# Kernel tuning notes

Hardware: AMD Instinct MI355X
Metric: run time of the kernel (lower is better)

The kernel has to match this reference:

```python
import jax, jax.numpy as jnp
import numpy as np

EMBED = 1024
HEADS = 16
HDIM = 64
FFN = 4 * EMBED
EPS = 1e-5


def setup_inputs() -> dict:
    key = jax.random.key(0)
    ks = jax.random.split(key, 12)
    def lin(k, fan_in, shape):
        b = 1.0 / np.sqrt(fan_in)
        return jax.random.uniform(k, shape, jnp.float32, -b, b)
    return {
        "x": jax.random.normal(ks[0], (4, 2048, EMBED), jnp.float32),
        "Wq": lin(ks[1], EMBED, (EMBED, HEADS * HDIM)),
        "Wk": lin(ks[2], EMBED, (EMBED, HEADS * HDIM)),
        "Wv": lin(ks[3], EMBED, (EMBED, HEADS * HDIM)),
        "Wo": lin(ks[4], HEADS * HDIM, (HEADS * HDIM, EMBED)),
        "ln1_g": jnp.ones((EMBED,), jnp.float32),
        "ln1_b": jnp.zeros((EMBED,), jnp.float32),
        "ln2_g": jnp.ones((EMBED,), jnp.float32),
        "ln2_b": jnp.zeros((EMBED,), jnp.float32),
        "W1": lin(ks[5], EMBED, (EMBED, FFN)),
        "b1": lin(ks[6], EMBED, (FFN,)),
        "W2": lin(ks[7], FFN, (FFN, EMBED)),
        "b2": lin(ks[8], FFN, (EMBED,)),
    }


def _layer_norm(x, g, b):
    mu = jnp.mean(x, axis=-1, keepdims=True)
    var = jnp.var(x, axis=-1, keepdims=True)
    return (x - mu) * jax.lax.rsqrt(var + EPS) * g + b


def reference(x, Wq, Wk, Wv, Wo, ln1_g, ln1_b, ln2_g, ln2_b, W1, b1, W2, b2):
    B, S, _ = x.shape
    residual = x
    h = _layer_norm(x, ln1_g, ln1_b)
    # project and split heads: [B, H, S, Dh]
    q = (h @ Wq).reshape(B, S, HEADS, HDIM).transpose(0, 2, 1, 3)
    k = (h @ Wk).reshape(B, S, HEADS, HDIM).transpose(0, 2, 1, 3)
    v = (h @ Wv).reshape(B, S, HEADS, HDIM).transpose(0, 2, 1, 3)
    scale = HDIM ** -0.5
    scores = jnp.einsum("bhqd,bhkd->bhqk", q, k) * scale
    # causal mask (upper triangle excluded above diagonal -> -inf)
    mask = jnp.triu(jnp.ones((S, S), bool), k=1)
    scores = jnp.where(mask, -jnp.inf, scores)
    attn = jax.nn.softmax(scores, axis=-1)
    out = jnp.einsum("bhqk,bhkd->bhqd", attn, v)
    out = out.transpose(0, 2, 1, 3).reshape(B, S, HEADS * HDIM)
    x = residual + out @ Wo
    residual = x
    h = _layer_norm(x, ln2_g, ln2_b)
    h = jax.nn.gelu(h @ W1 + b1, approximate=False) @ W2 + b2
    return residual + h
```

## Files before the change

kernel.cpp:

```cpp
#include <hip/hip_runtime.h>
#include <hip/hip_bf16.h>
#include <math.h>

typedef __bf16 bf16;
typedef bf16 bf16x8 __attribute__((ext_vector_type(8)));
typedef bf16 bf16x4 __attribute__((ext_vector_type(4)));
typedef float f32x4 __attribute__((ext_vector_type(4)));

#define ROWS 8192
#define EMB  1024
#define NH   16
#define HD   64
#define FFN  4096
#define QKVN 3072
#define SEQ  2048

__device__ __forceinline__ void gl2lds16(const bf16* g, bf16* l) {
  __builtin_amdgcn_global_load_lds((const __attribute__((address_space(1))) void*)g,
                                   (__attribute__((address_space(3))) void*)l, 16, 0, 0);
}

__global__ void transpose_cast(const float* __restrict__ W, bf16* __restrict__ Wt,
                               int K, int N, float scale) {
  __shared__ float tile[32][33];
  const int n0 = blockIdx.x * 32, k0 = blockIdx.y * 32;
  const int tx = threadIdx.x & 31, ty = threadIdx.x >> 5;
#pragma unroll
  for (int i = 0; i < 32; i += 8)
    tile[ty + i][tx] = W[(size_t)(k0 + ty + i) * N + n0 + tx];
  __syncthreads();
#pragma unroll
  for (int i = 0; i < 32; i += 8)
    Wt[(size_t)(n0 + ty + i) * K + k0 + tx] = (bf16)(tile[tx][ty + i] * scale);
}

__global__ void transpose_cast4(const float* __restrict__ W0, const float* __restrict__ W1,
                                const float* __restrict__ W2, const float* __restrict__ W3,
                                bf16* __restrict__ dst) {
  __shared__ float tile[32][33];
  const int z = blockIdx.z;
  const float* W = (z == 0) ? W0 : (z == 1) ? W1 : (z == 2) ? W2 : W3;
  const float scale = (z == 0) ? 0.125f : 1.0f;
  bf16* Wt = dst + (size_t)z * EMB * EMB;
  const int n0 = blockIdx.x * 32, k0 = blockIdx.y * 32;
  const int tx = threadIdx.x & 31, ty = threadIdx.x >> 5;
#pragma unroll
  for (int i = 0; i < 32; i += 8)
    tile[ty + i][tx] = W[(size_t)(k0 + ty + i) * EMB + n0 + tx];
  __syncthreads();
#pragma unroll
  for (int i = 0; i < 32; i += 8)
    Wt[(size_t)(n0 + ty + i) * EMB + k0 + tx] = (bf16)(tile[tx][ty + i] * scale);
}

__global__ void v_transpose(const bf16* __restrict__ qkv, bf16* __restrict__ vt) {
  __shared__ bf16 tile[32][33];
  const int s0 = blockIdx.x * 32, d0 = blockIdx.y * 32, bh = blockIdx.z;
  const int b = bh >> 4, h = bh & 15;
  const int tx = threadIdx.x & 31, ty = threadIdx.x >> 5;
#pragma unroll
  for (int i = 0; i < 32; i += 8)
    tile[ty + i][tx] = qkv[(size_t)(b * SEQ + s0 + ty + i) * QKVN + 2 * EMB + h * HD + d0 + tx];
  __syncthreads();
#pragma unroll
  for (int i = 0; i < 32; i += 8)
    vt[(size_t)(bh * HD + d0 + ty + i) * SEQ + s0 + tx] = tile[tx][ty + i];
}

__global__ __launch_bounds__(256) void layernorm_bf16(
    const float* __restrict__ x, const float* __restrict__ g,
    const float* __restrict__ b, bf16* __restrict__ out) {
  const int row = blockIdx.x * 4 + (threadIdx.x >> 6);
  const int lane = threadIdx.x & 63;
  const float4* xr = (const float4*)(x + (size_t)row * EMB);
  float4 v[4];
  float s = 0.f, ss = 0.f;
#pragma unroll
  for (int k = 0; k < 4; k++) {
    v[k] = xr[lane + 64 * k];
    s += v[k].x + v[k].y + v[k].z + v[k].w;
    ss += v[k].x * v[k].x + v[k].y * v[k].y + v[k].z * v[k].z + v[k].w * v[k].w;
  }
#pragma unroll
  for (int off = 32; off; off >>= 1) {
    s += __shfl_xor(s, off);
    ss += __shfl_xor(ss, off);
  }
  const float mu = s * (1.0f / EMB);
  const float rs = rsqrtf(ss * (1.0f / EMB) - mu * mu + 1e-5f);
  bf16* orow = out + (size_t)row * EMB;
#pragma unroll
  for (int k = 0; k < 4; k++) {
    const float4 gv = ((const float4*)g)[lane + 64 * k];
    const float4 bv = ((const float4*)b)[lane + 64 * k];
    bf16x4 o;
    o[0] = (bf16)((v[k].x - mu) * rs * gv.x + bv.x);
    o[1] = (bf16)((v[k].y - mu) * rs * gv.y + bv.y);
    o[2] = (bf16)((v[k].z - mu) * rs * gv.z + bv.z);
    o[3] = (bf16)((v[k].w - mu) * rs * gv.w + bv.w);
    *(bf16x4*)(orow + (size_t)(lane + 64 * k) * 4) = o;
  }
}

template <int EPI, int N_, int K_>
__global__ __launch_bounds__(256, 2) void gemm_bt(
    const bf16* __restrict__ A, const bf16* __restrict__ Bt, void* __restrict__ C,
    const float* __restrict__ bias, const float* __restrict__ resid) {
  constexpr int N = N_, K = K_;
  __shared__ __align__(16) bf16 As[128 * 64];
  __shared__ __align__(16) bf16 Bs[128 * 64];
  const int tid = threadIdx.x;
  const int lane = tid & 63;
  const int wave = tid >> 6;
  const int wm = (wave >> 1) * 64;
  const int wn = (wave & 1) * 64;
  constexpr int tn = N / 128;
  const int lin = blockIdx.y * tn + blockIdx.x;
  const int xcd = lin & 7;
  const int idx = lin >> 3;
  const int m0 = (xcd * 8 + (idx & 7)) * 128;
  const int n0 = (idx >> 3) * 128;
  const int quad = lane >> 4;
  const int l16 = lane & 15;
  const int srow8 = lane >> 3;
  const int scol = ((lane & 7) ^ srow8) * 8;
  const int xr = l16 & 7;

  const bf16* ap = A + (size_t)(m0 + wave * 32 + srow8) * K + scol;
  const bf16* bp = Bt + (size_t)(n0 + wave * 32 + srow8) * K + scol;
  bf16* const as0 = &As[wave * 32 * 64];
  bf16* const bs0 = &Bs[wave * 32 * 64];

  f32x4 acc[4][4] = {};

  for (int kt = 0; kt < K; kt += 64) {
    __syncthreads();
#pragma unroll
    for (int q = 0; q < 4; q++) {
      gl2lds16(ap + q * 8 * K, as0 + q * 8 * 64);
      gl2lds16(bp + q * 8 * K, bs0 + q * 8 * 64);
    }
    ap += 64;
    bp += 64;
    __syncthreads();
#pragma unroll
    for (int h = 0; h < 2; h++) {
      const int cp = ((h * 4 + quad) ^ xr) * 8;
      bf16x8 af[4], bfr[4];
#pragma unroll
      for (int i = 0; i < 4; i++)
        af[i] = *(const bf16x8*)&As[(wm + i * 16 + l16) * 64 + cp];
#pragma unroll
      for (int j = 0; j < 4; j++)
        bfr[j] = *(const bf16x8*)&Bs[(wn + j * 16 + l16) * 64 + cp];
#pragma unroll
      for (int i = 0; i < 4; i++)
#pragma unroll
        for (int j = 0; j < 4; j++)
          acc[i][j] = __builtin_amdgcn_mfma_f32_16x16x32_bf16(af[i], bfr[j], acc[i][j], 0, 0, 0);
    }
  }

#pragma unroll
  for (int i = 0; i < 4; i++)
#pragma unroll
    for (int j = 0; j < 4; j++)
#pragma unroll
      for (int r = 0; r < 4; r++) {
        const int row = m0 + wm + i * 16 + quad * 4 + r;
        const int col = n0 + wn + j * 16 + l16;
        const size_t idx2 = (size_t)row * N + col;
        float v = acc[i][j][r];
        if (EPI == 0) {
          ((bf16*)C)[idx2] = (bf16)v;
        } else if (EPI == 1) {
          ((float*)C)[idx2] = v + resid[idx2];
        } else if (EPI == 2) {
          v += bias[col];
          const float u = 1.5957691216f * (v + 0.044715f * v * v * v);
          v = v / (1.0f + __expf(-u));
          ((bf16*)C)[idx2] = (bf16)v;
        } else {
          ((float*)C)[idx2] = v + bias[col] + resid[idx2];
        }
      }
}

__global__ __launch_bounds__(256, 6) void flash_attn(
    const bf16* __restrict__ qkv, const bf16* __restrict__ vt, bf16* __restrict__ out) {
  const int bid = blockIdx.x;
  const int xcd = bid & 7;
  const int idx = bid >> 3;
  const int qt = 31 - (idx & 31);
  const int bh = xcd + ((idx >> 5) << 3);
  const int b = bh >> 4, h = bh & 15;
  const int tid = threadIdx.x;
  const int lane = tid & 63, wave = tid >> 6;
  const int quad = lane >> 4, l16 = lane & 15;

  __shared__ __align__(16) bf16 Ks[64 * 64];
  __shared__ __align__(16) bf16 Vts[64 * 64];
  __shared__ __align__(16) bf16 Ps[4][16][72];

  const size_t rowbase = (size_t)b * SEQ;
  const int s8 = (lane >> 3) & 7;
  const int cs = ((lane & 7) ^ s8) * 8;
  const int xk = l16 & 7;
  const bf16* kbase = qkv + rowbase * QKVN + EMB + h * HD;
  const bf16* vbase = vt + (size_t)(bh * HD) * SEQ;

  const int qrow_a = qt * 64 + wave * 16 + l16;
  const bf16* qptr = qkv + (rowbase + qrow_a) * QKVN + h * HD;
  const bf16x8 qf0 = *(const bf16x8*)(qptr + quad * 8);
  const bf16x8 qf1 = *(const bf16x8*)(qptr + 32 + quad * 8);
  f32x4 o0 = {}, o1 = {}, o2 = {}, o3 = {};
  f32x4 lsum = {};
  const int qrow_c = qt * 64 + wave * 16 + quad * 4;

  const bf16* kp = kbase + (size_t)(wave * 8 + s8) * QKVN + cs;
  const bf16* vp = vbase + (size_t)(wave * 8 + s8) * SEQ + cs;

#pragma unroll 1
  for (int kt = 0; kt <= qt; kt++) {
    __syncthreads();
    gl2lds16(kp + (size_t)kt * 64 * QKVN, &Ks[(wave * 8) * 64]);
    gl2lds16(kp + (size_t)(kt * 64 + 32) * QKVN, &Ks[(32 + wave * 8) * 64]);
    gl2lds16(vp + kt * 64, &Vts[(wave * 8) * 64]);
    gl2lds16(vp + (size_t)32 * SEQ + kt * 64, &Vts[(32 + wave * 8) * 64]);
    __syncthreads();

    if (kt < qt) {
#pragma unroll
      for (int j = 0; j < 4; j++) {
        const int rr = (j * 16 + l16) * 64;
        const bf16x8 kf0 = *(const bf16x8*)&Ks[rr + (quad ^ xk) * 8];
        const bf16x8 kf1 = *(const bf16x8*)&Ks[rr + ((4 + quad) ^ xk) * 8];
        f32x4 a = {};
        a = __builtin_amdgcn_mfma_f32_16x16x32_bf16(qf0, kf0, a, 0, 0, 0);
        a = __builtin_amdgcn_mfma_f32_16x16x32_bf16(qf1, kf1, a, 0, 0, 0);
#pragma unroll
        for (int r = 0; r < 4; r++) {
          const float pj = __expf(a[r]);
          lsum[r] += pj;
          Ps[wave][quad * 4 + r][j * 16 + l16] = (bf16)pj;
        }
      }
    } else {
#pragma unroll
      for (int j = 0; j < 4; j++) {
        if (j > wave) {
#pragma unroll
          for (int r = 0; r < 4; r++)
            Ps[wave][quad * 4 + r][j * 16 + l16] = (bf16)0.0f;
        } else {
          const int rr = (j * 16 + l16) * 64;
          const bf16x8 kf0 = *(const bf16x8*)&Ks[rr + (quad ^ xk) * 8];
          const bf16x8 kf1 = *(const bf16x8*)&Ks[rr + ((4 + quad) ^ xk) * 8];
          f32x4 a = {};
          a = __builtin_amdgcn_mfma_f32_16x16x32_bf16(qf0, kf0, a, 0, 0, 0);
          a = __builtin_amdgcn_mfma_f32_16x16x32_bf16(qf1, kf1, a, 0, 0, 0);
          if (j == wave) {
#pragma unroll
            for (int r = 0; r < 4; r++) {
              const float v = (l16 > quad * 4 + r) ? -INFINITY : a[r];
              const float pj = __expf(v);
              lsum[r] += pj;
              Ps[wave][quad * 4 + r][j * 16 + l16] = (bf16)pj;
            }
          } else {
#pragma unroll
            for (int r = 0; r < 4; r++) {
              const float pj = __expf(a[r]);
              lsum[r] += pj;
              Ps[wave][quad * 4 + r][j * 16 + l16] = (bf16)pj;
            }
          }
        }
      }
    }

    const bf16x8 af0 = *(const bf16x8*)&Ps[wave][l16][quad * 8];
    const bf16x8 af1 = *(const bf16x8*)&Ps[wave][l16][32 + quad * 8];
#pragma unroll
    for (int j = 0; j < 4; j++) {
      const int rr = (j * 16 + l16) * 64;
      const bf16x8 vf0 = *(const bf16x8*)&Vts[rr + (quad ^ xk) * 8];
      const bf16x8 vf1 = *(const bf16x8*)&Vts[rr + ((4 + quad) ^ xk) * 8];
      f32x4& oj = (j == 0) ? o0 : (j == 1) ? o1 : (j == 2) ? o2 : o3;
      oj = __builtin_amdgcn_mfma_f32_16x16x32_bf16(af0, vf0, oj, 0, 0, 0);
      oj = __builtin_amdgcn_mfma_f32_16x16x32_bf16(af1, vf1, oj, 0, 0, 0);
    }
  }

#pragma unroll
  for (int r = 0; r < 4; r++) {
    float ls = lsum[r];
    ls += __shfl_xor(ls, 1);
    ls += __shfl_xor(ls, 2);
    ls += __shfl_xor(ls, 4);
    ls += __shfl_xor(ls, 8);
    const float iv = 1.0f / ls;
    bf16* op = out + (rowbase + qrow_c + r) * EMB + h * HD;
    op[0 + l16] = (bf16)(o0[r] * iv);
    op[16 + l16] = (bf16)(o1[r] * iv);
    op[32 + l16] = (bf16)(o2[r] * iv);
    op[48 + l16] = (bf16)(o3[r] * iv);
  }
}

extern "C" void kernel_launch(void* const* d_in, const int* in_sizes, int n_in,
                              void* d_out, int out_size, void* d_ws, size_t ws_size,
                              hipStream_t stream) {
  const float* x     = (const float*)d_in[0];
  const float* Wq    = (const float*)d_in[1];
  const float* Wk    = (const float*)d_in[2];
  const float* Wv    = (const float*)d_in[3];
  const float* Wo    = (const float*)d_in[4];
  const float* ln1_g = (const float*)d_in[5];
  const float* ln1_b = (const float*)d_in[6];
  const float* ln2_g = (const float*)d_in[7];
  const float* ln2_b = (const float*)d_in[8];
  const float* W1    = (const float*)d_in[9];
  const float* b1    = (const float*)d_in[10];
  const float* W2    = (const float*)d_in[11];
  const float* b2    = (const float*)d_in[12];
  float* out = (float*)d_out;

  bf16* p = (bf16*)d_ws;
  bf16* wqkv_t = p;                 p += (size_t)QKVN * EMB;
  bf16* wo_t   = p;                 p += (size_t)EMB * EMB;
  bf16* w1_t   = p;                 p += (size_t)FFN * EMB;
  bf16* w2_t   = p;                 p += (size_t)EMB * FFN;
  bf16* h      = p;                 p += (size_t)ROWS * EMB;
  bf16* qkv    = p;                 p += (size_t)ROWS * QKVN;
  bf16* attn_o = p;                 p += (size_t)ROWS * EMB;
  bf16* ffn1   = p;
  bf16* vt     = h;

  transpose_cast4<<<dim3(32, 32, 4), 256, 0, stream>>>(Wq, Wk, Wv, Wo, wqkv_t);
  transpose_cast<<<dim3(128, 32), 256, 0, stream>>>(W1, w1_t, EMB, FFN, 1.0f);
  transpose_cast<<<dim3(32, 128), 256, 0, stream>>>(W2, w2_t, FFN, EMB, 1.0f);

  layernorm_bf16<<<ROWS / 4, 256, 0, stream>>>(x, ln1_g, ln1_b, h);

  gemm_bt<0, QKVN, EMB><<<dim3(QKVN / 128, ROWS / 128), 256, 0, stream>>>(
      h, wqkv_t, qkv, nullptr, nullptr);

  v_transpose<<<dim3(SEQ / 32, HD / 32, 64), 256, 0, stream>>>(qkv, vt);

  flash_attn<<<2048, 256, 0, stream>>>(qkv, vt, attn_o);

  gemm_bt<1, EMB, EMB><<<dim3(EMB / 128, ROWS / 128), 256, 0, stream>>>(
      attn_o, wo_t, out, nullptr, x);

  layernorm_bf16<<<ROWS / 4, 256, 0, stream>>>(out, ln2_g, ln2_b, h);

  gemm_bt<2, FFN, EMB><<<dim3(FFN / 128, ROWS / 128), 256, 0, stream>>>(
      h, w1_t, ffn1, b1, nullptr);

  gemm_bt<3, EMB, FFN><<<dim3(EMB / 128, ROWS / 128), 256, 0, stream>>>(
      ffn1, w2_t, out, b2, out);
}
```

Measured before the change: 481.0 us.

## Pair causal q-tiles per block, double-buffer K in LDS, read V from global

Each attention block now processes two query tiles (qt and 31-qt) so every block does a balanced amount of causal work, and the grid is halved accordingly. K tiles are double-buffered in LDS with the next tile prefetched while the current one is used. V fragments are loaded directly from global memory instead of being staged in LDS. This aims to remove tail imbalance and load stalls, at the risk of uncoalesced, latency-bound V reads and fewer resident blocks.

```diff
diff --git a/kernel.cpp b/kernel.cpp
--- a/kernel.cpp
+++ b/kernel.cpp
@@ -191,15 +191,14 @@
   const int bid = blockIdx.x;
   const int xcd = bid & 7;
   const int idx = bid >> 3;
-  const int qt = 31 - (idx & 31);
-  const int bh = xcd + ((idx >> 5) << 3);
+  const int pr = idx & 15;
+  const int bh = xcd + ((idx >> 4) << 3);
   const int b = bh >> 4, h = bh & 15;
   const int tid = threadIdx.x;
   const int lane = tid & 63, wave = tid >> 6;
   const int quad = lane >> 4, l16 = lane & 15;
 
-  __shared__ __align__(16) bf16 Ks[64 * 64];
-  __shared__ __align__(16) bf16 Vts[64 * 64];
+  __shared__ __align__(16) bf16 Ks[2][64 * 64];
   __shared__ __align__(16) bf16 Ps[4][16][72];
 
   const size_t rowbase = (size_t)b * SEQ;
@@ -209,103 +208,115 @@
   const bf16* kbase = qkv + rowbase * QKVN + EMB + h * HD;
   const bf16* vbase = vt + (size_t)(bh * HD) * SEQ;
 
-  const int qrow_a = qt * 64 + wave * 16 + l16;
-  const bf16* qptr = qkv + (rowbase + qrow_a) * QKVN + h * HD;
-  const bf16x8 qf0 = *(const bf16x8*)(qptr + quad * 8);
-  const bf16x8 qf1 = *(const bf16x8*)(qptr + 32 + quad * 8);
-  f32x4 o0 = {}, o1 = {}, o2 = {}, o3 = {};
-  f32x4 lsum = {};
-  const int qrow_c = qt * 64 + wave * 16 + quad * 4;
-
   const bf16* kp = kbase + (size_t)(wave * 8 + s8) * QKVN + cs;
-  const bf16* vp = vbase + (size_t)(wave * 8 + s8) * SEQ + cs;
+
+#define STAGE_K(BUF, T)                                                        \
+  gl2lds16(kp + (size_t)(T) * 64 * QKVN, &Ks[(BUF)][(wave * 8) * 64]);         \
+  gl2lds16(kp + ((size_t)(T) * 64 + 32) * QKVN, &Ks[(BUF)][(32 + wave * 8) * 64]);
 
 #pragma unroll 1
-  for (int kt = 0; kt <= qt; kt++) {
-    __syncthreads();
-    gl2lds16(kp + (size_t)kt * 64 * QKVN, &Ks[(wave * 8) * 64]);
-    gl2lds16(kp + (size_t)(kt * 64 + 32) * QKVN, &Ks[(32 + wave * 8) * 64]);
-    gl2lds16(vp + kt * 64, &Vts[(wave * 8) * 64]);
-    gl2lds16(vp + (size_t)32 * SEQ + kt * 64, &Vts[(32 + wave * 8) * 64]);
-    __syncthreads();
-
-    if (kt < qt) {
-#pragma unroll
-      for (int j = 0; j < 4; j++) {
-        const int rr = (j * 16 + l16) * 64;
-        const bf16x8 kf0 = *(const bf16x8*)&Ks[rr + (quad ^ xk) * 8];
-        const bf16x8 kf1 = *(const bf16x8*)&Ks[rr + ((4 + quad) ^ xk) * 8];
-        f32x4 a = {};
-        a = __builtin_amdgcn_mfma_f32_16x16x32_bf16(qf0, kf0, a, 0, 0, 0);
-        a = __builtin_amdgcn_mfma_f32_16x16x32_bf16(qf1, kf1, a, 0, 0, 0);
-#pragma unroll
-        for (int r = 0; r < 4; r++) {
-          const float pj = __expf(a[r]);
-          lsum[r] += pj;
-          Ps[wave][quad * 4 + r][j * 16 + l16] = (bf16)pj;
-        }
-      }
-    } else {
-#pragma unroll
-      for (int j = 0; j < 4; j++) {
-        if (j > wave) {
-#pragma unroll
-          for (int r = 0; r < 4; r++)
-            Ps[wave][quad * 4 + r][j * 16 + l16] = (bf16)0.0f;
-        } else {
+  for (int half = 0; half < 2; half++) {
+    const int qt = half ? pr : 31 - pr;
+    const int qrow_a = qt * 64 + wave * 16 + l16;
+    const bf16* qptr = qkv + (rowbase + qrow_a) * QKVN + h * HD;
+    const bf16x8 qf0 = *(const bf16x8*)(qptr + quad * 8);
+    const bf16x8 qf1 = *(const bf16x8*)(qptr + 32 + quad * 8);
+    f32x4 o0 = {}, o1 = {}, o2 = {}, o3 = {};
+    f32x4 lsum = {};
+    const int qrow_c = qt * 64 + wave * 16 + quad * 4;
+
+    STAGE_K(0, 0);
+    asm volatile("s_waitcnt vmcnt(0)");
+    __builtin_amdgcn_s_barrier();
+
+#pragma unroll 1
+    for (int kt = 0; kt <= qt; kt++) {
+      const int cb = kt & 1;
+      if (kt < qt) { STAGE_K(cb ^ 1, kt + 1); }
+      const bf16* Kc = &Ks[cb][0];
+
+      if (kt < qt) {
+#pragma unroll
+        for (int j = 0; j < 4; j++) {
           const int rr = (j * 16 + l16) * 64;
-          const bf16x8 kf0 = *(const bf16x8*)&Ks[rr + (quad ^ xk) * 8];
-          const bf16x8 kf1 = *(const bf16x8*)&Ks[rr + ((4 + quad) ^ xk) * 8];
+          const bf16x8 kf0 = *(const bf16x8*)&Kc[rr + (quad ^ xk) * 8];
+          const bf16x8 kf1 = *(const bf16x8*)&Kc[rr + ((4 + quad) ^ xk) * 8];
           f32x4 a = {};
           a = __builtin_amdgcn_mfma_f32_16x16x32_bf16(qf0, kf0, a, 0, 0, 0);
           a = __builtin_amdgcn_mfma_f32_16x16x32_bf16(qf1, kf1, a, 0, 0, 0);
-          if (j == wave) {
-#pragma unroll
-            for (int r = 0; r < 4; r++) {
-              const float v = (l16 > quad * 4 + r) ? -INFINITY : a[r];
-              const float pj = __expf(v);
-              lsum[r] += pj;
-              Ps[wave][quad * 4 + r][j * 16 + l16] = (bf16)pj;
-            }
+#pragma unroll
+          for (int r = 0; r < 4; r++) {
+            const float pj = __expf(a[r]);
+            lsum[r] += pj;
+            Ps[wave][quad * 4 + r][j * 16 + l16] = (bf16)pj;
+          }
+        }
+      } else {
+#pragma unroll
+        for (int j = 0; j < 4; j++) {
+          if (j > wave) {
+#pragma unroll
+            for (int r = 0; r < 4; r++)
+              Ps[wave][quad * 4 + r][j * 16 + l16] = (bf16)0.0f;
           } else {
-#pragma unroll
-            for (int r = 0; r < 4; r++) {
-              const float pj = __expf(a[r]);
-              lsum[r] += pj;
-              Ps[wave][quad * 4 + r][j * 16 + l16] = (bf16)pj;
+            const int rr = (j * 16 + l16) * 64;
+            const bf16x8 kf0 = *(const bf16x8*)&Kc[rr + (quad ^ xk) * 8];
+            const bf16x8 kf1 = *(const bf16x8*)&Kc[rr + ((4 + quad) ^ xk) * 8];
+            f32x4 a = {};
+            a = __builtin_amdgcn_mfma_f32_16x16x32_bf16(qf0, kf0, a, 0, 0, 0);
+            a = __builtin_amdgcn_mfma_f32_16x16x32_bf16(qf1, kf1, a, 0, 0, 0);
+            if (j == wave) {
+#pragma unroll
+              for (int r = 0; r < 4; r++) {
+                const float v = (l16 > quad * 4 + r) ? -INFINITY : a[r];
+                const float pj = __expf(v);
+                lsum[r] += pj;
+                Ps[wave][quad * 4 + r][j * 16 + l16] = (bf16)pj;
+              }
+            } else {
+#pragma unroll
+              for (int r = 0; r < 4; r++) {
+                const float pj = __expf(a[r]);
+                lsum[r] += pj;
+                Ps[wave][quad * 4 + r][j * 16 + l16] = (bf16)pj;
+              }
             }
           }
         }
       }
+
+      const bf16x8 af0 = *(const bf16x8*)&Ps[wave][l16][quad * 8];
+      const bf16x8 af1 = *(const bf16x8*)&Ps[wave][l16][32 + quad * 8];
+#pragma unroll
+      for (int j = 0; j < 4; j++) {
+        const bf16* vrow = vbase + (size_t)(j * 16 + l16) * SEQ + kt * 64;
+        const bf16x8 vf0 = *(const bf16x8*)(vrow + quad * 8);
+        const bf16x8 vf1 = *(const bf16x8*)(vrow + 32 + quad * 8);
+        f32x4& oj = (j == 0) ? o0 : (j == 1) ? o1 : (j == 2) ? o2 : o3;
+        oj = __builtin_amdgcn_mfma_f32_16x16x32_bf16(af0, vf0, oj, 0, 0, 0);
+        oj = __builtin_amdgcn_mfma_f32_16x16x32_bf16(af1, vf1, oj, 0, 0, 0);
+      }
+
+      asm volatile("s_waitcnt vmcnt(0)");
+      __builtin_amdgcn_s_barrier();
     }
 
-    const bf16x8 af0 = *(const bf16x8*)&Ps[wave][l16][quad * 8];
-    const bf16x8 af1 = *(const bf16x8*)&Ps[wave][l16][32 + quad * 8];
-#pragma unroll
-    for (int j = 0; j < 4; j++) {
-      const int rr = (j * 16 + l16) * 64;
-      const bf16x8 vf0 = *(const bf16x8*)&Vts[rr + (quad ^ xk) * 8];
-      const bf16x8 vf1 = *(const bf16x8*)&Vts[rr + ((4 + quad) ^ xk) * 8];
-      f32x4& oj = (j == 0) ? o0 : (j == 1) ? o1 : (j == 2) ? o2 : o3;
-      oj = __builtin_amdgcn_mfma_f32_16x16x32_bf16(af0, vf0, oj, 0, 0, 0);
-      oj = __builtin_amdgcn_mfma_f32_16x16x32_bf16(af1, vf1, oj, 0, 0, 0);
+#pragma unroll
+    for (int r = 0; r < 4; r++) {
+      float ls = lsum[r];
+      ls += __shfl_xor(ls, 1);
+      ls += __shfl_xor(ls, 2);
+      ls += __shfl_xor(ls, 4);
+      ls += __shfl_xor(ls, 8);
+      const float iv = 1.0f / ls;
+      bf16* op = out + (rowbase + qrow_c + r) * EMB + h * HD;
+      op[0 + l16] = (bf16)(o0[r] * iv);
+      op[16 + l16] = (bf16)(o1[r] * iv);
+      op[32 + l16] = (bf16)(o2[r] * iv);
+      op[48 + l16] = (bf16)(o3[r] * iv);
     }
   }
-
-#pragma unroll
-  for (int r = 0; r < 4; r++) {
-    float ls = lsum[r];
-    ls += __shfl_xor(ls, 1);
-    ls += __shfl_xor(ls, 2);
-    ls += __shfl_xor(ls, 4);
-    ls += __shfl_xor(ls, 8);
-    const float iv = 1.0f / ls;
-    bf16* op = out + (rowbase + qrow_c + r) * EMB + h * HD;
-    op[0 + l16] = (bf16)(o0[r] * iv);
-    op[16 + l16] = (bf16)(o1[r] * iv);
-    op[32 + l16] = (bf16)(o2[r] * iv);
-    op[48 + l16] = (bf16)(o3[r] * iv);
-  }
+#undef STAGE_K
 }
 
 extern "C" void kernel_launch(void* const* d_in, const int* in_sizes, int n_in,
@@ -348,7 +359,7 @@
 
   v_transpose<<<dim3(SEQ / 32, HD / 32, 64), 256, 0, stream>>>(qkv, vt);
 
-  flash_attn<<<2048, 256, 0, stream>>>(qkv, vt, attn_o);
+  flash_attn<<<1024, 256, 0, stream>>>(qkv, vt, attn_o);
 
   gemm_bt<1, EMB, EMB><<<dim3(EMB / 128, ROWS / 128), 256, 0, stream>>>(
       attn_o, wo_t, out, nullptr, x);
```

New measurement: 511.8 us. +6.4%, slower.

## Pair causal query tiles per block and register-prefetch next K/V tile

Applied to the files above, without the earlier changes.

Each flash-attention block now processes two query tiles (qt and 31-qt) so every block does equal causal work, halving the grid. K/V loads switch from direct global-to-LDS copies to register staging, and the next tile is loaded while the current one is computed, overlapping global latency with MFMA work. The cost is higher register pressure and fewer blocks, which may reduce occupancy and tail parallelism.

```diff
diff --git a/kernel.cpp b/kernel.cpp
--- a/kernel.cpp
+++ b/kernel.cpp
@@ -191,8 +191,8 @@
   const int bid = blockIdx.x;
   const int xcd = bid & 7;
   const int idx = bid >> 3;
-  const int qt = 31 - (idx & 31);
-  const int bh = xcd + ((idx >> 5) << 3);
+  const int pr = idx & 15;
+  const int bh = xcd + ((idx >> 4) << 3);
   const int b = bh >> 4, h = bh & 15;
   const int tid = threadIdx.x;
   const int lane = tid & 63, wave = tid >> 6;
@@ -209,103 +209,125 @@
   const bf16* kbase = qkv + rowbase * QKVN + EMB + h * HD;
   const bf16* vbase = vt + (size_t)(bh * HD) * SEQ;
 
-  const int qrow_a = qt * 64 + wave * 16 + l16;
-  const bf16* qptr = qkv + (rowbase + qrow_a) * QKVN + h * HD;
-  const bf16x8 qf0 = *(const bf16x8*)(qptr + quad * 8);
-  const bf16x8 qf1 = *(const bf16x8*)(qptr + 32 + quad * 8);
-  f32x4 o0 = {}, o1 = {}, o2 = {}, o3 = {};
-  f32x4 lsum = {};
-  const int qrow_c = qt * 64 + wave * 16 + quad * 4;
-
   const bf16* kp = kbase + (size_t)(wave * 8 + s8) * QKVN + cs;
   const bf16* vp = vbase + (size_t)(wave * 8 + s8) * SEQ + cs;
+  bf16* const kd0 = &Ks[(wave * 8) * 64 + lane * 8];
+  bf16* const kd1 = &Ks[(32 + wave * 8) * 64 + lane * 8];
+  bf16* const vd0 = &Vts[(wave * 8) * 64 + lane * 8];
+  bf16* const vd1 = &Vts[(32 + wave * 8) * 64 + lane * 8];
+
+  bf16x8 rk0, rk1, rv0, rv1;
+#define LOAD_KV(T)                                                             \
+  rk0 = *(const bf16x8*)(kp + (size_t)(T) * 64 * QKVN);                        \
+  rk1 = *(const bf16x8*)(kp + ((size_t)(T) * 64 + 32) * QKVN);                 \
+  rv0 = *(const bf16x8*)(vp + (T) * 64);                                       \
+  rv1 = *(const bf16x8*)(vp + (size_t)32 * SEQ + (T) * 64);
 
 #pragma unroll 1
-  for (int kt = 0; kt <= qt; kt++) {
-    __syncthreads();
-    gl2lds16(kp + (size_t)kt * 64 * QKVN, &Ks[(wave * 8) * 64]);
-    gl2lds16(kp + (size_t)(kt * 64 + 32) * QKVN, &Ks[(32 + wave * 8) * 64]);
-    gl2lds16(vp + kt * 64, &Vts[(wave * 8) * 64]);
-    gl2lds16(vp + (size_t)32 * SEQ + kt * 64, &Vts[(32 + wave * 8) * 64]);
-    __syncthreads();
-
-    if (kt < qt) {
-#pragma unroll
-      for (int j = 0; j < 4; j++) {
-        const int rr = (j * 16 + l16) * 64;
-        const bf16x8 kf0 = *(const bf16x8*)&Ks[rr + (quad ^ xk) * 8];
-        const bf16x8 kf1 = *(const bf16x8*)&Ks[rr + ((4 + quad) ^ xk) * 8];
-        f32x4 a = {};
-        a = __builtin_amdgcn_mfma_f32_16x16x32_bf16(qf0, kf0, a, 0, 0, 0);
-        a = __builtin_amdgcn_mfma_f32_16x16x32_bf16(qf1, kf1, a, 0, 0, 0);
-#pragma unroll
-        for (int r = 0; r < 4; r++) {
-          const float pj = __expf(a[r]);
-          lsum[r] += pj;
-          Ps[wave][quad * 4 + r][j * 16 + l16] = (bf16)pj;
-        }
-      }
-    } else {
-#pragma unroll
-      for (int j = 0; j < 4; j++) {
-        if (j > wave) {
-#pragma unroll
-          for (int r = 0; r < 4; r++)
-            Ps[wave][quad * 4 + r][j * 16 + l16] = (bf16)0.0f;
-        } else {
+  for (int half = 0; half < 2; half++) {
+    const int qt = half ? pr : 31 - pr;
+    const int qrow_a = qt * 64 + wave * 16 + l16;
+    const bf16* qptr = qkv + (rowbase + qrow_a) * QKVN + h * HD;
+    const bf16x8 qf0 = *(const bf16x8*)(qptr + quad * 8);
+    const bf16x8 qf1 = *(const bf16x8*)(qptr + 32 + quad * 8);
+    f32x4 o0 = {}, o1 = {}, o2 = {}, o3 = {};
+    f32x4 lsum = {};
+    const int qrow_c = qt * 64 + wave * 16 + quad * 4;
+
+    LOAD_KV(0);
+
+#pragma unroll 1
+    for (int kt = 0; kt <= qt; kt++) {
+      __builtin_amdgcn_sched_barrier(0);
+      __builtin_amdgcn_s_barrier();
+      *(bf16x8*)kd0 = rk0;
+      *(bf16x8*)kd1 = rk1;
+      *(bf16x8*)vd0 = rv0;
+      *(bf16x8*)vd1 = rv1;
+      if (kt < qt) { LOAD_KV(kt + 1); }
+      asm volatile("s_waitcnt lgkmcnt(0)");
+      __builtin_amdgcn_sched_barrier(0);
+      __builtin_amdgcn_s_barrier();
+
+      if (kt < qt) {
+#pragma unroll
+        for (int j = 0; j < 4; j++) {
           const int rr = (j * 16 + l16) * 64;
           const bf16x8 kf0 = *(const bf16x8*)&Ks[rr + (quad ^ xk) * 8];
           const bf16x8 kf1 = *(const bf16x8*)&Ks[rr + ((4 + quad) ^ xk) * 8];
           f32x4 a = {};
           a = __builtin_amdgcn_mfma_f32_16x16x32_bf16(qf0, kf0, a, 0, 0, 0);
           a = __builtin_amdgcn_mfma_f32_16x16x32_bf16(qf1, kf1, a, 0, 0, 0);
-          if (j == wave) {
-#pragma unroll
-            for (int r = 0; r < 4; r++) {
-              const float v = (l16 > quad * 4 + r) ? -INFINITY : a[r];
-              const float pj = __expf(v);
-              lsum[r] += pj;
-              Ps[wave][quad * 4 + r][j * 16 + l16] = (bf16)pj;
-            }
+#pragma unroll
+          for (int r = 0; r < 4; r++) {
+            const float pj = __expf(a[r]);
+            lsum[r] += pj;
+            Ps[wave][quad * 4 + r][j * 16 + l16] = (bf16)pj;
+          }
+        }
+      } else {
+#pragma unroll
+        for (int j = 0; j < 4; j++) {
+          if (j > wave) {
+#pragma unroll
+            for (int r = 0; r < 4; r++)
+              Ps[wave][quad * 4 + r][j * 16 + l16] = (bf16)0.0f;
           } else {
-#pragma unroll
-            for (int r = 0; r < 4; r++) {
-              const float pj = __expf(a[r]);
-              lsum[r] += pj;
-              Ps[wave][quad * 4 + r][j * 16 + l16] = (bf16)pj;
+            const int rr = (j * 16 + l16) * 64;
+            const bf16x8 kf0 = *(const bf16x8*)&Ks[rr + (quad ^ xk) * 8];
+            const bf16x8 kf1 = *(const bf16x8*)&Ks[rr + ((4 + quad) ^ xk) * 8];
+            f32x4 a = {};
+            a = __builtin_amdgcn_mfma_f32_16x16x32_bf16(qf0, kf0, a, 0, 0, 0);
+            a = __builtin_amdgcn_mfma_f32_16x16x32_bf16(qf1, kf1, a, 0, 0, 0);
+            if (j == wave) {
+#pragma unroll
+              for (int r = 0; r < 4; r++) {
+                const float v = (l16 > quad * 4 + r) ? -INFINITY : a[r];
+                const float pj = __expf(v);
+                lsum[r] += pj;
+                Ps[wave][quad * 4 + r][j * 16 + l16] = (bf16)pj;
+              }
+            } else {
+#pragma unroll
+              for (int r = 0; r < 4; r++) {
+                const float pj = __expf(a[r]);
+                lsum[r] += pj;
+                Ps[wave][quad * 4 + r][j * 16 + l16] = (bf16)pj;
+              }
             }
           }
         }
       }
+
+      const bf16x8 af0 = *(const bf16x8*)&Ps[wave][l16][quad * 8];
+      const bf16x8 af1 = *(const bf16x8*)&Ps[wave][l16][32 + quad * 8];
+#pragma unroll
+      for (int j = 0; j < 4; j++) {
+        const int rr = (j * 16 + l16) * 64;
+        const bf16x8 vf0 = *(const bf16x8*)&Vts[rr + (quad ^ xk) * 8];
+        const bf16x8 vf1 = *(const bf16x8*)&Vts[rr + ((4 + quad) ^ xk) * 8];
+        f32x4& oj = (j == 0) ? o0 : (j == 1) ? o1 : (j == 2) ? o2 : o3;
+        oj = __builtin_amdgcn_mfma_f32_16x16x32_bf16(af0, vf0, oj, 0, 0, 0);
+        oj = __builtin_amdgcn_mfma_f32_16x16x32_bf16(af1, vf1, oj, 0, 0, 0);
+      }
     }
 
-    const bf16x8 af0 = *(const bf16x8*)&Ps[wave][l16][quad * 8];
-    const bf16x8 af1 = *(const bf16x8*)&Ps[wave][l16][32 + quad * 8];
-#pragma unroll
-    for (int j = 0; j < 4; j++) {
-      const int rr = (j * 16 + l16) * 64;
-      const bf16x8 vf0 = *(const bf16x8*)&Vts[rr + (quad ^ xk) * 8];
-      const bf16x8 vf1 = *(const bf16x8*)&Vts[rr + ((4 + quad) ^ xk) * 8];
-      f32x4& oj = (j == 0) ? o0 : (j == 1) ? o1 : (j == 2) ? o2 : o3;
-      oj = __builtin_amdgcn_mfma_f32_16x16x32_bf16(af0, vf0, oj, 0, 0, 0);
-      oj = __builtin_amdgcn_mfma_f32_16x16x32_bf16(af1, vf1, oj, 0, 0, 0);
+#pragma unroll
+    for (int r = 0; r < 4; r++) {
+      float ls = lsum[r];
+      ls += __shfl_xor(ls, 1);
+      ls += __shfl_xor(ls, 2);
+      ls += __shfl_xor(ls, 4);
+      ls += __shfl_xor(ls, 8);
+      const float iv = 1.0f / ls;
+      bf16* op = out + (rowbase + qrow_c + r) * EMB + h * HD;
+      op[0 + l16] = (bf16)(o0[r] * iv);
+      op[16 + l16] = (bf16)(o1[r] * iv);
+      op[32 + l16] = (bf16)(o2[r] * iv);
+      op[48 + l16] = (bf16)(o3[r] * iv);
     }
   }
-
-#pragma unroll
-  for (int r = 0; r < 4; r++) {
-    float ls = lsum[r];
-    ls += __shfl_xor(ls, 1);
-    ls += __shfl_xor(ls, 2);
-    ls += __shfl_xor(ls, 4);
-    ls += __shfl_xor(ls, 8);
-    const float iv = 1.0f / ls;
-    bf16* op = out + (rowbase + qrow_c + r) * EMB + h * HD;
-    op[0 + l16] = (bf16)(o0[r] * iv);
-    op[16 + l16] = (bf16)(o1[r] * iv);
-    op[32 + l16] = (bf16)(o2[r] * iv);
-    op[48 + l16] = (bf16)(o3[r] * iv);
-  }
+#undef LOAD_KV
 }
 
 extern "C" void kernel_launch(void* const* d_in, const int* in_sizes, int n_in,
@@ -348,7 +370,7 @@
 
   v_transpose<<<dim3(SEQ / 32, HD / 32, 64), 256, 0, stream>>>(qkv, vt);
 
-  flash_attn<<<2048, 256, 0, stream>>>(qkv, vt, attn_o);
+  flash_attn<<<1024, 256, 0, stream>>>(qkv, vt, attn_o);
 
   gemm_bt<1, EMB, EMB><<<dim3(EMB / 128, ROWS / 128), 256, 0, stream>>>(
       attn_o, wo_t, out, nullptr, x);
```

Result: slower. 539.3 us (+12.1%).
